# Optimization experiments

Measured on AMD Instinct MI355X. Metric: run time of the kernel, lower is better.

Reference implementation:

```python
import jax, jax.numpy as jnp
import numpy as np

ALPHA = 0.25
GAMMA = 2.0
LAMBDA_T = 0.1


def count_components(fg):
    """Count 6-connected components per volume. fg: [M,H,W,D] bool.
    Min-label propagation + pointer jumping (parallel union-find style CCL),
    matching scipy.ndimage.label's default face-connectivity structure.
    Returns float32 [M] component counts."""
    M, H, W, D = fg.shape
    N = H * W * D
    BIG = jnp.int32(N)  # sentinel label for background / padding
    idx = jnp.arange(N, dtype=jnp.int32).reshape(1, H, W, D)
    L0 = jnp.broadcast_to(idx, fg.shape)

    def shift(a, axis, d):
        # b[i] = a[i-d] along `axis`, padded with BIG outside the volume
        pad = [(0, 0)] * 4
        pad[axis] = (max(d, 0), max(-d, 0))
        ap = jnp.pad(a, pad, constant_values=N)
        sl = [slice(None)] * 4
        sl[axis] = slice(max(-d, 0), max(-d, 0) + a.shape[axis])
        return ap[tuple(sl)]

    def one_step(L):
        Lv = jnp.where(fg, L, BIG)
        m = Lv
        for ax in (1, 2, 3):
            for d in (1, -1):
                m = jnp.minimum(m, shift(Lv, ax, d))
        Ln = jnpp_min = jnp.where(fg, jnp.minimum(L, m), L)
        # pointer jumping (L <- L[L]) twice for log-depth convergence
        Lf = Ln.reshape(M, N)
        Lf = jnp.take_along_axis(Lf, Lf, axis=1)
        Lf = jnp.take_along_axis(Lf, Lf, axis=1)
        return Lf.reshape(M, H, W, D)

    def cond(s):
        return s[1]

    def body(s):
        L, _ = s
        Ln = one_step(L)
        return (Ln, jnp.any(Ln != L))

    L, _ = jax.lax.while_loop(cond, body, (L0, jnp.bool_(True)))
    # at fixed point every foreground component carries its min linear index;
    # roots satisfy L[i] == i
    roots = fg & (L == idx)
    return jnp.sum(roots, axis=(1, 2, 3)).astype(jnp.float32)


def _focal(x, t):
    p = jax.nn.sigmoid(x)
    pt = jnp.where(t == 1, p, 1.0 - p)
    bce = jax.nn.softplus(x) - x * t  # BCE-with-logits, elementwise
    alpha_t = jnp.where(t == 1, ALPHA, 1.0 - ALPHA)
    return jnp.mean(alpha_t * (1.0 - pt) ** GAMMA * bce)


def _topology(x, t):
    B, C = x.shape[:2]
    spatial = x.shape[2:]
    fg_p = (jax.nn.sigmoid(x) > 0.5).reshape(B * C, *spatial)
    fg_t = (t > 0.5).reshape(B * C, *spatial)
    cc_p = count_components(fg_p).reshape(B, C).mean(axis=0)  # mean over batch per class
    cc_t = count_components(fg_t).reshape(B, C).mean(axis=0)
    return jnp.mean(jnp.abs(cc_p - cc_t))  # sum over classes / C


def setup_inputs() -> dict:
    key = jax.random.key(0)
    k1, k2 = jax.random.split(key)
    shape = (2, 2, 96, 96, 96)
    pred_logits = jax.random.normal(k1, shape, dtype=jnp.float32)
    target_binary = jax.random.randint(k2, shape, 0, 2).astype(jnp.float32)
    return {"pred_logits": pred_logits, "target_binary": target_binary}


def reference(pred_logits, target_binary):
    focal = _focal(pred_logits, target_binary)
    topo = jax.lax.stop_gradient(_topology(pred_logits, target_binary))
    return focal + LAMBDA_T * topo
```

## Files before the change

### kernel.cpp

```cpp
#include <hip/hip_runtime.h>
#include <math.h>

#define N_VOX (96*96*96)
#define NVOL 8
#define NEL (4*N_VOX)
#define PLANE (96*96)

#define TW 8
#define TH 8
#define TILES_W 12
#define TILES_H 12
#define TILE_VOX (96*TW*TH)
#define TILE_WORDS (TILE_VOX/32)
#define MAXRUNS 3072

#define NBPLANES 11
#define NPAIRS (2*NBPLANES)
#define FACES_PER_VOL (2*NPAIRS*PLANE)
#define MAXR 40192
#define FALLR 65536
#define SEGCAP 4608
#define HT2N 4096
#define MAX_PROBES 16

#define WS_ACC   0
#define WS_ROOT  256
#define WS_EVT   1536
#define WS_PCNT  2816
#define WS_HDR   4096

__device__ __forceinline__ int uf_find(int* __restrict__ L, int x) {
    int r = x;
    int p = L[r];
    while (p != r) { r = p; p = L[r]; }
    if (r != x) atomicMin(&L[x], r);
    return r;
}

__device__ __forceinline__ int uf_merge(int* __restrict__ L, int l1, int l2) {
    int ev = 0;
    while (l1 != l2) {
        if (l1 < l2) { int t = l1; l1 = l2; l2 = t; }
        int l3 = atomicMin(&L[l1], l2);
        if (l3 == l1) { ev++; l1 = l2; }
        else l1 = l3;
    }
    return ev;
}

__device__ __forceinline__ void merge_local(int* lab, int l1, int l2) {
    while (l1 != l2 && l1 != lab[l1]) l1 = lab[l1];
    while (l1 != l2 && l2 != lab[l2]) l2 = lab[l2];
    while (l1 != l2) {
        if (l1 < l2) { int t = l1; l1 = l2; l2 = t; }
        int l3 = atomicMin(&lab[l1], l2);
        l1 = (l3 == l1) ? l2 : l3;
    }
}

__device__ __forceinline__ int rrank(const unsigned* __restrict__ sm,
                                     const int* __restrict__ wpf, int i) {
    int w = i >> 5, b = i & 31;
    unsigned mask = (2u << b) - 1u;
    return wpf[w] + __popc(sm[w] & mask) - 1;
}

__global__ __launch_bounds__(256) void ccl_local(const float* __restrict__ pred,
                                                 const float* __restrict__ targ,
                                                 unsigned short* __restrict__ faces,
                                                 int* __restrict__ rootcnt,
                                                 float* __restrict__ acc,
                                                 int vbase) {
    __shared__ int      lab[MAXRUNS];
    __shared__ unsigned fm[TILE_WORDS];
    __shared__ unsigned sm[TILE_WORDS];
    __shared__ int      wpf[TILE_WORDS];
    __shared__ float fws[4];
    __shared__ int   iws[4];
    __shared__ int   gbase;

    int vloc = blockIdx.y;
    int v = vbase + vloc;
    int tile = blockIdx.x;
    int tw = tile % TILES_W, th = tile / TILES_W;
    int w0 = tw * TW, h0 = th * TH;
    int tbase = h0 * PLANE + w0 * 96;
    unsigned short* Fw = faces + (size_t)vloc * FACES_PER_VOL;
    unsigned short* Fh = Fw + 2 * NBPLANES * PLANE;

    float fsum = 0.0f;
    for (int it = 0; it < TILE_VOX / 256; it++) {
        int i = it * 256 + threadIdx.x;
        int lh = i / 768;
        int j = tbase + i + lh * 8448;
        bool f;
        if (v < 4) {
            float xv = pred[(size_t)v * N_VOX + j];
            float tv = targ[(size_t)v * N_VOX + j];
            f = xv > 0.0f;
            float m   = (tv == 1.0f) ? -xv : xv;
            float at  = (tv == 1.0f) ? 0.25f : 0.75f;
            float e   = __expf(-fabsf(m));
            float inv = 1.0f / (1.0f + e);
            float sig = inv * ((m >= 0.0f) ? 1.0f : e);
            float sp  = fmaxf(m, 0.0f) + __logf(1.0f + e);
            fsum += at * sig * sig * sp;
        } else {
            f = targ[(size_t)(v - 4) * N_VOX + j] > 0.5f;
        }
        unsigned long long bal = __ballot(f);
        if ((threadIdx.x & 63) == 0) {
            fm[i >> 5]       = (unsigned)bal;
            fm[(i >> 5) + 1] = (unsigned)(bal >> 32);
        }
    }
    __syncthreads();

    int cnt = 0;
    {
        unsigned st = 0;
        if (threadIdx.x < TILE_WORDS) {
            unsigned m = fm[threadIdx.x];
            unsigned carry = (threadIdx.x % 3) ? (fm[threadIdx.x - 1] >> 31) : 0u;
            st = m & ~((m << 1) | carry);
            sm[threadIdx.x] = st;
            cnt = __popc(st);
        }
    }
    int inc = cnt;
    for (int off = 1; off < 64; off <<= 1) {
        int u = __shfl_up(inc, off, 64);
        if ((threadIdx.x & 63) >= off) inc += u;
    }
    int wid = threadIdx.x >> 6;
    if ((threadIdx.x & 63) == 63) iws[wid] = inc;
    for (int r = threadIdx.x; r < MAXRUNS; r += 256) lab[r] = r;
    __syncthreads();
    int woff = 0;
    for (int k = 0; k < wid; k++) woff += iws[k];
    if (threadIdx.x < TILE_WORDS) wpf[threadIdx.x] = woff + inc - cnt;
    int Nr = iws[0] + iws[1] + iws[2];
    __syncthreads();

    for (int t = threadIdx.x; t < 336; t += 256) {
        bool wdirn = t < 168;
        int tt = wdirn ? t : t - 168;
        int lh, lw, k;
        if (wdirn) { lh = tt / 21; int rem = tt % 21; lw = rem / 3; k = rem % 3; }
        else       { lh = tt / 24; int rem = tt % 24; lw = rem / 3; k = rem % 3; }
        int wb = (lh * 8 + lw) * 3 + k;
        int nb = wb + (wdirn ? 3 : 24);
        unsigned ov = fm[wb] & fm[nb];
        if (!ov) continue;
        unsigned carry = (k > 0) ? ((fm[wb - 1] & fm[nb - 1]) >> 31) : 0u;
        unsigned starts = ov & ~((ov << 1) | carry);
        int base_i = wb << 5;
        int dir = wdirn ? 96 : 768;
        while (starts) {
            int b = __builtin_ctz(starts);
            starts &= starts - 1;
            int i = base_i + b;
            merge_local(lab, rrank(sm, wpf, i), rrank(sm, wpf, i + dir));
        }
    }
    __syncthreads();

    int myroots = 0;
    for (int r = threadIdx.x; r < Nr; r += 256)
        if (lab[r] == r) myroots++;
    int s = myroots;
    for (int off = 1; off < 64; off <<= 1) {
        int u = __shfl_up(s, off, 64);
        if ((threadIdx.x & 63) >= off) s += u;
    }
    if ((threadIdx.x & 63) == 63) iws[wid] = s;
    __syncthreads();
    int wbase = 0;
    for (int k = 0; k < wid; k++) wbase += iws[k];
    if (threadIdx.x == 0)
        gbase = atomicAdd(&rootcnt[v << 5], iws[0] + iws[1] + iws[2] + iws[3]);
    __syncthreads();
    int nid = gbase + wbase + (s - myroots);
    for (int r = threadIdx.x; r < Nr; r += 256)
        if (lab[r] == r) lab[r] = ~(nid++);
    __syncthreads();

    for (int r = threadIdx.x; r < Nr; r += 256) {
        int p = lab[r];
        if (p >= 0) {
            int q2 = lab[p];
            while (q2 >= 0) { p = q2; q2 = lab[p]; }
            lab[r] = q2;
        }
    }
    __syncthreads();

    for (int t = threadIdx.x; t < 768; t += 256) {
        int f  = t / 192;
        int g  = t % 192;
        int u  = g / 24;
        int d4 = (g % 24) * 4;
        int i0; unsigned short* dst;
        if (f == 0) {
            if (tw == 0) continue;
            i0  = u * 768 + d4;
            dst = Fw + ((tw - 1) * 2 + 1) * PLANE + (h0 + u) * 96 + d4;
        } else if (f == 1) {
            if (tw == TILES_W - 1) continue;
            i0  = u * 768 + 7 * 96 + d4;
            dst = Fw + (tw * 2) * PLANE + (h0 + u) * 96 + d4;
        } else if (f == 2) {
            if (th == 0) continue;
            i0  = u * 96 + d4;
            dst = Fh + ((th - 1) * 2 + 1) * PLANE + (w0 + u) * 96 + d4;
        } else {
            if (th == TILES_H - 1) continue;
            i0  = 7 * 768 + u * 96 + d4;
            dst = Fh + (th * 2) * PLANE + (w0 + u) * 96 + d4;
        }
        unsigned mw = fm[i0 >> 5];
        unsigned short vals[4];
        bool prevf = false;
        for (int q = 0; q < 4; q++) {
            bool fb = (mw >> ((d4 & 31) + q)) & 1;
            if (fb) vals[q] = prevf ? vals[q - 1]
                                    : (unsigned short)(~lab[rrank(sm, wpf, i0 + q)]);
            else vals[q] = 0xFFFFu;
            prevf = fb;
        }
        *(ushort4*)dst = make_ushort4(vals[0], vals[1], vals[2], vals[3]);
    }

    for (int off = 32; off; off >>= 1) fsum += __shfl_down(fsum, off, 64);
    if ((threadIdx.x & 63) == 0) fws[wid] = fsum;
    __syncthreads();
    if (threadIdx.x == 0) {
        float ft = fws[0] + fws[1] + fws[2] + fws[3];
        if (v < 4 && ft != 0.0f) atomicAdd(acc, ft);
    }
}

__global__ __launch_bounds__(256) void ccl_pairs(const unsigned short* __restrict__ faces,
                                                 unsigned* __restrict__ pairs,
                                                 int* __restrict__ pcnt,
                                                 int vbase) {
    __shared__ unsigned ht[HT2N];
    __shared__ int nloc;
    for (int i = threadIdx.x; i < HT2N; i += 256) ht[i] = 0xFFFFFFFFu;
    if (threadIdx.x == 0) nloc = 0;
    __syncthreads();

    int f    = blockIdx.x;
    int vloc = blockIdx.y;
    int v    = vbase + vloc;
    const unsigned short* A = faces + (size_t)vloc * FACES_PER_VOL
                                    + (size_t)(2 * f) * PLANE;
    const unsigned short* B = A + PLANE;
    unsigned* pb = pairs + ((size_t)vloc * NPAIRS + f) * SEGCAP;

    const int GPP = PLANE / 8;
    for (int g = threadIdx.x; g < GPP; g += 256) {
        int e8 = g * 8;
        int4 aw = *(const int4*)(A + e8);
        int4 bw = *(const int4*)(B + e8);
        unsigned a32[4] = {(unsigned)aw.x, (unsigned)aw.y, (unsigned)aw.z, (unsigned)aw.w};
        unsigned b32[4] = {(unsigned)bw.x, (unsigned)bw.y, (unsigned)bw.z, (unsigned)bw.w};
        bool pf = false;
        if (e8 % 96) pf = (A[e8 - 1] != 0xFFFFu) && (B[e8 - 1] != 0xFFFFu);
        #pragma unroll
        for (int q = 0; q < 8; q++) {
            unsigned av = (a32[q >> 1] >> ((q & 1) * 16)) & 0xFFFFu;
            unsigned bv = (b32[q >> 1] >> ((q & 1) * 16)) & 0xFFFFu;
            bool f2 = (av != 0xFFFFu) && (bv != 0xFFFFu);
            if (f2 && !pf && av != bv) {
                unsigned lo = av < bv ? av : bv;
                unsigned hi = av < bv ? bv : av;
                unsigned key = (lo << 16) | hi;
                unsigned h = (key * 2654435761u) >> 20;
                bool fresh = false;
                for (int pr = 0; pr < MAX_PROBES; pr++) {
                    unsigned prev = atomicCAS(&ht[h], 0xFFFFFFFFu, key);
                    if (prev == 0xFFFFFFFFu) { fresh = true; break; }
                    if (prev == key) break;
                    h = (h + 1) & (HT2N - 1);
                    if (pr == MAX_PROBES - 1) fresh = true;
                }
                if (fresh) {
                    int ix = atomicAdd(&nloc, 1);
                    pb[ix] = key;
                }
            }
            pf = f2;
        }
    }
    __syncthreads();
    if (threadIdx.x == 0) pcnt[v * NPAIRS + f] = nloc;
}

__global__ __launch_bounds__(1024) void ccl_union(const unsigned* __restrict__ pairs,
                                                  int* __restrict__ gfall,
                                                  const int* __restrict__ rootcnt,
                                                  const int* __restrict__ pcnt,
                                                  int* __restrict__ events,
                                                  int vbase) {
    __shared__ int slab[MAXR];
    __shared__ int wsum[16];
    int vloc = blockIdx.x;
    int v = vbase + vloc;
    int R  = rootcnt[v << 5];

    int* lab = (R <= MAXR) ? (int*)slab : (gfall + (size_t)vloc * FALLR);
    for (int i = threadIdx.x; i < R; i += 1024) lab[i] = i;
    __syncthreads();

    int ev = 0;
    for (int f = 0; f < NPAIRS; f++) {
        int np = pcnt[v * NPAIRS + f];
        const unsigned* pb = pairs + ((size_t)vloc * NPAIRS + f) * SEGCAP;
        for (int i = threadIdx.x; i < np; i += 1024) {
            unsigned key = pb[i];
            int a = (int)(key >> 16), b = (int)(key & 0xFFFFu);
            int ra = uf_find(lab, a);
            int rb = uf_find(lab, b);
            if (ra != rb) ev += uf_merge(lab, ra, rb);
        }
    }

    for (int off = 32; off; off >>= 1) ev += __shfl_down(ev, off, 64);
    if ((threadIdx.x & 63) == 0) wsum[threadIdx.x >> 6] = ev;
    __syncthreads();
    if (threadIdx.x == 0) {
        int tot = 0;
        for (int k = 0; k < 16; k++) tot += wsum[k];
        events[v << 5] = tot;
    }
}

__global__ void finalize_kernel(const float* __restrict__ acc,
                                const int* __restrict__ rootcnt,
                                const int* __restrict__ events,
                                float* __restrict__ out) {
    float focal = acc[0] / (float)NEL;
    float c[NVOL];
    for (int v = 0; v < NVOL; v++)
        c[v] = (float)(rootcnt[v << 5] - events[v << 5]);
    float dp0 = 0.5f * (c[0] + c[2]);
    float dp1 = 0.5f * (c[1] + c[3]);
    float dt0 = 0.5f * (c[4] + c[6]);
    float dt1 = 0.5f * (c[5] + c[7]);
    float topo = 0.5f * (fabsf(dp0 - dt0) + fabsf(dp1 - dt1));
    out[0] = focal + 0.1f * topo;
}

extern "C" void kernel_launch(void* const* d_in, const int* in_sizes, int n_in,
                              void* d_out, int out_size, void* d_ws, size_t ws_size,
                              hipStream_t stream) {
    const float* pred = (const float*)d_in[0];
    const float* targ = (const float*)d_in[1];
    float* out = (float*)d_out;

    float* acc     = (float*)((char*)d_ws + WS_ACC);
    int*   rootcnt = (int*)((char*)d_ws + WS_ROOT);
    int*   events  = (int*)((char*)d_ws + WS_EVT);
    int*   pcnt    = (int*)((char*)d_ws + WS_PCNT);
    unsigned short* faces = (unsigned short*)((char*)d_ws + WS_HDR);

    size_t per_vol = (size_t)FACES_PER_VOL * 2
                   + (size_t)NPAIRS * SEGCAP * 4
                   + (size_t)FALLR * 4;
    size_t avail   = (ws_size > WS_HDR) ? ws_size - WS_HDR : 0;
    int vols_per_pass = (int)(avail / per_vol);
    if (vols_per_pass > NVOL) vols_per_pass = NVOL;
    if (vols_per_pass < 1) vols_per_pass = 1;
    unsigned* pairs = (unsigned*)(faces + (size_t)vols_per_pass * FACES_PER_VOL);
    int* gfall = (int*)(pairs + (size_t)vols_per_pass * NPAIRS * SEGCAP);

    hipMemsetAsync(d_ws, 0, WS_HDR, stream);

    for (int vbase = 0; vbase < NVOL; vbase += vols_per_pass) {
        int nv = NVOL - vbase;
        if (nv > vols_per_pass) nv = vols_per_pass;
        dim3 tgrid(TILES_W * TILES_H, nv);
        ccl_local<<<tgrid, dim3(256), 0, stream>>>(pred, targ, faces,
                                                   rootcnt, acc, vbase);
        dim3 pgrid(NPAIRS, nv);
        ccl_pairs<<<pgrid, dim3(256), 0, stream>>>(faces, pairs, pcnt, vbase);
        ccl_union<<<dim3(nv), dim3(1024), 0, stream>>>(pairs, gfall, rootcnt,
                                                       pcnt, events, vbase);
    }

    finalize_kernel<<<1, 1, 0, stream>>>(acc, rootcnt, events, out);
}
```

Before: 162.1 us.

## Fuse boundary pair extraction with global union-find using atomic global labels

Removes the separate pair-buffer and single-block-per-volume union kernel. Each face-pair block now deduplicates label pairs locally and immediately performs lock-free union-find merges on a global label array, which ccl_local initialises for each new root. This trades shared-memory union work in one large block per volume for parallel global-memory atomics across many blocks, and removes one launch plus the pair buffer traffic.

```diff
diff --git a/kernel.cpp b/kernel.cpp
--- a/kernel.cpp
+++ b/kernel.cpp
@@ -17,16 +17,13 @@
 #define NBPLANES 11
 #define NPAIRS (2*NBPLANES)
 #define FACES_PER_VOL (2*NPAIRS*PLANE)
-#define MAXR 40192
 #define FALLR 65536
-#define SEGCAP 4608
 #define HT2N 4096
 #define MAX_PROBES 16
 
 #define WS_ACC   0
 #define WS_ROOT  256
 #define WS_EVT   1536
-#define WS_PCNT  2816
 #define WS_HDR   4096
 
 __device__ __forceinline__ int uf_find(int* __restrict__ L, int x) {
@@ -68,6 +65,7 @@
 __global__ __launch_bounds__(256) void ccl_local(const float* __restrict__ pred,
                                                  const float* __restrict__ targ,
                                                  unsigned short* __restrict__ faces,
+                                                 int* __restrict__ gfall,
                                                  int* __restrict__ rootcnt,
                                                  float* __restrict__ acc,
                                                  int vbase) {
@@ -87,6 +85,7 @@
     int tbase = h0 * PLANE + w0 * 96;
     unsigned short* Fw = faces + (size_t)vloc * FACES_PER_VOL;
     unsigned short* Fh = Fw + 2 * NBPLANES * PLANE;
+    int* Gv = gfall + (size_t)vloc * FALLR;
 
     float fsum = 0.0f;
     for (int it = 0; it < TILE_VOX / 256; it++) {
@@ -182,7 +181,7 @@
     __syncthreads();
     int nid = gbase + wbase + (s - myroots);
     for (int r = threadIdx.x; r < Nr; r += 256)
-        if (lab[r] == r) lab[r] = ~(nid++);
+        if (lab[r] == r) { Gv[nid] = nid; lab[r] = ~(nid++); }
     __syncthreads();
 
     for (int r = threadIdx.x; r < Nr; r += 256) {
@@ -240,14 +239,13 @@
     }
 }
 
-__global__ __launch_bounds__(256) void ccl_pairs(const unsigned short* __restrict__ faces,
-                                                 unsigned* __restrict__ pairs,
-                                                 int* __restrict__ pcnt,
+__global__ __launch_bounds__(256) void ccl_merge(const unsigned short* __restrict__ faces,
+                                                 int* __restrict__ gfall,
+                                                 int* __restrict__ events,
                                                  int vbase) {
     __shared__ unsigned ht[HT2N];
-    __shared__ int nloc;
+    __shared__ int wsum[4];
     for (int i = threadIdx.x; i < HT2N; i += 256) ht[i] = 0xFFFFFFFFu;
-    if (threadIdx.x == 0) nloc = 0;
     __syncthreads();
 
     int f    = blockIdx.x;
@@ -256,8 +254,9 @@
     const unsigned short* A = faces + (size_t)vloc * FACES_PER_VOL
                                     + (size_t)(2 * f) * PLANE;
     const unsigned short* B = A + PLANE;
-    unsigned* pb = pairs + ((size_t)vloc * NPAIRS + f) * SEGCAP;
-
+    int* L = gfall + (size_t)vloc * FALLR;
+
+    int ev = 0;
     const int GPP = PLANE / 8;
     for (int g = threadIdx.x; g < GPP; g += 256) {
         int e8 = g * 8;
@@ -286,53 +285,21 @@
                     if (pr == MAX_PROBES - 1) fresh = true;
                 }
                 if (fresh) {
-                    int ix = atomicAdd(&nloc, 1);
-                    pb[ix] = key;
+                    int ra = uf_find(L, (int)lo);
+                    int rb = uf_find(L, (int)hi);
+                    if (ra != rb) ev += uf_merge(L, ra, rb);
                 }
             }
             pf = f2;
         }
     }
-    __syncthreads();
-    if (threadIdx.x == 0) pcnt[v * NPAIRS + f] = nloc;
-}
-
-__global__ __launch_bounds__(1024) void ccl_union(const unsigned* __restrict__ pairs,
-                                                  int* __restrict__ gfall,
-                                                  const int* __restrict__ rootcnt,
-                                                  const int* __restrict__ pcnt,
-                                                  int* __restrict__ events,
-                                                  int vbase) {
-    __shared__ int slab[MAXR];
-    __shared__ int wsum[16];
-    int vloc = blockIdx.x;
-    int v = vbase + vloc;
-    int R  = rootcnt[v << 5];
-
-    int* lab = (R <= MAXR) ? (int*)slab : (gfall + (size_t)vloc * FALLR);
-    for (int i = threadIdx.x; i < R; i += 1024) lab[i] = i;
-    __syncthreads();
-
-    int ev = 0;
-    for (int f = 0; f < NPAIRS; f++) {
-        int np = pcnt[v * NPAIRS + f];
-        const unsigned* pb = pairs + ((size_t)vloc * NPAIRS + f) * SEGCAP;
-        for (int i = threadIdx.x; i < np; i += 1024) {
-            unsigned key = pb[i];
-            int a = (int)(key >> 16), b = (int)(key & 0xFFFFu);
-            int ra = uf_find(lab, a);
-            int rb = uf_find(lab, b);
-            if (ra != rb) ev += uf_merge(lab, ra, rb);
-        }
-    }
 
     for (int off = 32; off; off >>= 1) ev += __shfl_down(ev, off, 64);
     if ((threadIdx.x & 63) == 0) wsum[threadIdx.x >> 6] = ev;
     __syncthreads();
     if (threadIdx.x == 0) {
-        int tot = 0;
-        for (int k = 0; k < 16; k++) tot += wsum[k];
-        events[v << 5] = tot;
+        int tot = wsum[0] + wsum[1] + wsum[2] + wsum[3];
+        if (tot) atomicAdd(&events[v << 5], tot);
     }
 }
 
@@ -362,18 +329,14 @@
     float* acc     = (float*)((char*)d_ws + WS_ACC);
     int*   rootcnt = (int*)((char*)d_ws + WS_ROOT);
     int*   events  = (int*)((char*)d_ws + WS_EVT);
-    int*   pcnt    = (int*)((char*)d_ws + WS_PCNT);
     unsigned short* faces = (unsigned short*)((char*)d_ws + WS_HDR);
 
-    size_t per_vol = (size_t)FACES_PER_VOL * 2
-                   + (size_t)NPAIRS * SEGCAP * 4
-                   + (size_t)FALLR * 4;
+    size_t per_vol = (size_t)FACES_PER_VOL * 2 + (size_t)FALLR * 4;
     size_t avail   = (ws_size > WS_HDR) ? ws_size - WS_HDR : 0;
     int vols_per_pass = (int)(avail / per_vol);
     if (vols_per_pass > NVOL) vols_per_pass = NVOL;
     if (vols_per_pass < 1) vols_per_pass = 1;
-    unsigned* pairs = (unsigned*)(faces + (size_t)vols_per_pass * FACES_PER_VOL);
-    int* gfall = (int*)(pairs + (size_t)vols_per_pass * NPAIRS * SEGCAP);
+    int* gfall = (int*)(faces + (size_t)vols_per_pass * FACES_PER_VOL);
 
     hipMemsetAsync(d_ws, 0, WS_HDR, stream);
 
@@ -381,12 +344,10 @@
         int nv = NVOL - vbase;
         if (nv > vols_per_pass) nv = vols_per_pass;
         dim3 tgrid(TILES_W * TILES_H, nv);
-        ccl_local<<<tgrid, dim3(256), 0, stream>>>(pred, targ, faces,
+        ccl_local<<<tgrid, dim3(256), 0, stream>>>(pred, targ, faces, gfall,
                                                    rootcnt, acc, vbase);
-        dim3 pgrid(NPAIRS, nv);
-        ccl_pairs<<<pgrid, dim3(256), 0, stream>>>(faces, pairs, pcnt, vbase);
-        ccl_union<<<dim3(nv), dim3(1024), 0, stream>>>(pairs, gfall, rootcnt,
-                                                       pcnt, events, vbase);
+        dim3 mgrid(NPAIRS, nv);
+        ccl_merge<<<mgrid, dim3(256), 0, stream>>>(faces, gfall, events, vbase);
     }
 
     finalize_kernel<<<1, 1, 0, stream>>>(acc, rootcnt, events, out);
```

Result: slower. 193.2 us (+19.2%).

## Fuse pair extraction, union-find merge and finalize into one last-block-done kernel

Applied to the files above, without the earlier changes.

Merges the pair-extraction, union and finalize kernels into a single launch. Each (face, volume) block extracts its pairs, and the last block to finish for a volume, detected through an atomic counter, runs the union-find over all pairs. The last volume to finish then computes the final loss. This removes two kernel launches and their inter-kernel gaps. The union loop is also flattened across faces with prefix offsets, and the pair stage now uses 1024-thread blocks that share the large LDS label buffer, which limits occupancy during the pair stage.

```diff
diff --git a/kernel.cpp b/kernel.cpp
--- a/kernel.cpp
+++ b/kernel.cpp
@@ -25,9 +25,11 @@
 
 #define WS_ACC   0
 #define WS_ROOT  256
-#define WS_EVT   1536
-#define WS_PCNT  2816
-#define WS_HDR   4096
+#define WS_COMP  1536
+#define WS_DONE  2816
+#define WS_VDONE 3840
+#define WS_PCNT  4096
+#define WS_HDR   8192
 
 __device__ __forceinline__ int uf_find(int* __restrict__ L, int x) {
     int r = x;
@@ -240,15 +242,22 @@
     }
 }
 
-__global__ __launch_bounds__(256) void ccl_pairs(const unsigned short* __restrict__ faces,
-                                                 unsigned* __restrict__ pairs,
-                                                 int* __restrict__ pcnt,
-                                                 int vbase) {
-    __shared__ unsigned ht[HT2N];
-    __shared__ int nloc;
-    for (int i = threadIdx.x; i < HT2N; i += 256) ht[i] = 0xFFFFFFFFu;
-    if (threadIdx.x == 0) nloc = 0;
-    __syncthreads();
+__global__ __launch_bounds__(1024) void ccl_bmerge(const unsigned short* __restrict__ faces,
+                                                   unsigned* __restrict__ pairs,
+                                                   int* __restrict__ pcnt,
+                                                   int* __restrict__ gfall,
+                                                   const int* __restrict__ rootcnt,
+                                                   int* __restrict__ comp,
+                                                   int* __restrict__ done,
+                                                   int* __restrict__ vdone,
+                                                   const float* __restrict__ acc,
+                                                   float* __restrict__ out,
+                                                   int vbase) {
+    __shared__ int slab[MAXR];
+    __shared__ int offs[NPAIRS + 1];
+    __shared__ int wsum[16];
+    __shared__ int nloc, lastf, lastv;
+    unsigned* ht = (unsigned*)slab;
 
     int f    = blockIdx.x;
     int vloc = blockIdx.y;
@@ -258,8 +267,12 @@
     const unsigned short* B = A + PLANE;
     unsigned* pb = pairs + ((size_t)vloc * NPAIRS + f) * SEGCAP;
 
+    for (int i = threadIdx.x; i < HT2N; i += 1024) ht[i] = 0xFFFFFFFFu;
+    if (threadIdx.x == 0) nloc = 0;
+    __syncthreads();
+
     const int GPP = PLANE / 8;
-    for (int g = threadIdx.x; g < GPP; g += 256) {
+    for (int g = threadIdx.x; g < GPP; g += 1024) {
         int e8 = g * 8;
         int4 aw = *(const int4*)(A + e8);
         int4 bw = *(const int4*)(B + e8);
@@ -294,62 +307,64 @@
         }
     }
     __syncthreads();
-    if (threadIdx.x == 0) pcnt[v * NPAIRS + f] = nloc;
-}
-
-__global__ __launch_bounds__(1024) void ccl_union(const unsigned* __restrict__ pairs,
-                                                  int* __restrict__ gfall,
-                                                  const int* __restrict__ rootcnt,
-                                                  const int* __restrict__ pcnt,
-                                                  int* __restrict__ events,
-                                                  int vbase) {
-    __shared__ int slab[MAXR];
-    __shared__ int wsum[16];
-    int vloc = blockIdx.x;
-    int v = vbase + vloc;
-    int R  = rootcnt[v << 5];
-
-    int* lab = (R <= MAXR) ? (int*)slab : (gfall + (size_t)vloc * FALLR);
+    if (threadIdx.x == 0) {
+        pcnt[v * NPAIRS + f] = nloc;
+        __threadfence();
+        int old = atomicAdd(&done[v << 5], 1);
+        lastf = (old == NPAIRS - 1);
+    }
+    __syncthreads();
+    if (!lastf) return;
+
+    __threadfence();
+    int R = rootcnt[v << 5];
+    int* lab = (R <= MAXR) ? slab : (gfall + (size_t)vloc * FALLR);
+    if (threadIdx.x == 0) {
+        int o = 0;
+        for (int k = 0; k < NPAIRS; k++) { offs[k] = o; o += pcnt[v * NPAIRS + k]; }
+        offs[NPAIRS] = o;
+    }
+    __syncthreads();
     for (int i = threadIdx.x; i < R; i += 1024) lab[i] = i;
+    int tot = offs[NPAIRS];
     __syncthreads();
 
     int ev = 0;
-    for (int f = 0; f < NPAIRS; f++) {
-        int np = pcnt[v * NPAIRS + f];
-        const unsigned* pb = pairs + ((size_t)vloc * NPAIRS + f) * SEGCAP;
-        for (int i = threadIdx.x; i < np; i += 1024) {
-            unsigned key = pb[i];
-            int a = (int)(key >> 16), b = (int)(key & 0xFFFFu);
-            int ra = uf_find(lab, a);
-            int rb = uf_find(lab, b);
-            if (ra != rb) ev += uf_merge(lab, ra, rb);
-        }
+    for (int gi = threadIdx.x; gi < tot; gi += 1024) {
+        int fi = 0;
+        while (offs[fi + 1] <= gi) fi++;
+        unsigned key = pairs[((size_t)vloc * NPAIRS + fi) * SEGCAP + (gi - offs[fi])];
+        int a = (int)(key >> 16), b = (int)(key & 0xFFFFu);
+        int ra = uf_find(lab, a);
+        int rb = uf_find(lab, b);
+        if (ra != rb) ev += uf_merge(lab, ra, rb);
     }
 
     for (int off = 32; off; off >>= 1) ev += __shfl_down(ev, off, 64);
     if ((threadIdx.x & 63) == 0) wsum[threadIdx.x >> 6] = ev;
     __syncthreads();
     if (threadIdx.x == 0) {
-        int tot = 0;
-        for (int k = 0; k < 16; k++) tot += wsum[k];
-        events[v << 5] = tot;
-    }
-}
-
-__global__ void finalize_kernel(const float* __restrict__ acc,
-                                const int* __restrict__ rootcnt,
-                                const int* __restrict__ events,
-                                float* __restrict__ out) {
-    float focal = acc[0] / (float)NEL;
-    float c[NVOL];
-    for (int v = 0; v < NVOL; v++)
-        c[v] = (float)(rootcnt[v << 5] - events[v << 5]);
-    float dp0 = 0.5f * (c[0] + c[2]);
-    float dp1 = 0.5f * (c[1] + c[3]);
-    float dt0 = 0.5f * (c[4] + c[6]);
-    float dt1 = 0.5f * (c[5] + c[7]);
-    float topo = 0.5f * (fabsf(dp0 - dt0) + fabsf(dp1 - dt1));
-    out[0] = focal + 0.1f * topo;
+        int tote = 0;
+        for (int k = 0; k < 16; k++) tote += wsum[k];
+        comp[v << 5] = R - tote;
+        __threadfence();
+        int old2 = atomicAdd(vdone, 1);
+        lastv = (old2 == NVOL - 1);
+    }
+    __syncthreads();
+    if (!lastv) return;
+
+    if (threadIdx.x == 0) {
+        __threadfence();
+        float c[NVOL];
+        for (int w = 0; w < NVOL; w++) c[w] = (float)comp[w << 5];
+        float dp0 = 0.5f * (c[0] + c[2]);
+        float dp1 = 0.5f * (c[1] + c[3]);
+        float dt0 = 0.5f * (c[4] + c[6]);
+        float dt1 = 0.5f * (c[5] + c[7]);
+        float topo = 0.5f * (fabsf(dp0 - dt0) + fabsf(dp1 - dt1));
+        out[0] = acc[0] / (float)NEL + 0.1f * topo;
+    }
 }
 
 extern "C" void kernel_launch(void* const* d_in, const int* in_sizes, int n_in,
@@ -361,7 +376,9 @@
 
     float* acc     = (float*)((char*)d_ws + WS_ACC);
     int*   rootcnt = (int*)((char*)d_ws + WS_ROOT);
-    int*   events  = (int*)((char*)d_ws + WS_EVT);
+    int*   comp    = (int*)((char*)d_ws + WS_COMP);
+    int*   done    = (int*)((char*)d_ws + WS_DONE);
+    int*   vdone   = (int*)((char*)d_ws + WS_VDONE);
     int*   pcnt    = (int*)((char*)d_ws + WS_PCNT);
     unsigned short* faces = (unsigned short*)((char*)d_ws + WS_HDR);
 
@@ -383,11 +400,9 @@
         dim3 tgrid(TILES_W * TILES_H, nv);
         ccl_local<<<tgrid, dim3(256), 0, stream>>>(pred, targ, faces,
                                                    rootcnt, acc, vbase);
-        dim3 pgrid(NPAIRS, nv);
-        ccl_pairs<<<pgrid, dim3(256), 0, stream>>>(faces, pairs, pcnt, vbase);
-        ccl_union<<<dim3(nv), dim3(1024), 0, stream>>>(pairs, gfall, rootcnt,
-                                                       pcnt, events, vbase);
-    }
-
-    finalize_kernel<<<1, 1, 0, stream>>>(acc, rootcnt, events, out);
-}
+        dim3 mgrid(NPAIRS, nv);
+        ccl_bmerge<<<mgrid, dim3(1024), 0, stream>>>(faces, pairs, pcnt, gfall,
+                                                     rootcnt, comp, done, vdone,
+                                                     acc, out, vbase);
+    }
+}
```

Measured after the change: 151.9 us. -6.3%, faster.
